# Optimization experiments

Hardware: AMD Instinct MI355X
Metric: run time of the kernel (lower is better)

Reference implementation:

```python
import jax, jax.numpy as jnp
import numpy as np

R = 8
INPUT_DIM = 2048
OUTPUT_DIM = 2048
SCALING = 16.0 / R  # lora_alpha / r
TEMPERATURE = 1.0
LN_EPS = 1e-5


def setup_inputs() -> dict:
    key = jax.random.key(0)
    ks = jax.random.split(key, 6)
    bs, seq, ctr_out, ctr_final = 8, 2048, 32, 4
    x = jax.random.normal(ks[0], (bs, seq, INPUT_DIM), dtype=jnp.float32)
    ctr = jax.random.normal(ks[1], (bs, ctr_out), dtype=jnp.float32)
    W1 = jax.random.normal(ks[2], (60, ctr_out), dtype=jnp.float32) * (1.0 / np.sqrt(ctr_out))
    b1 = jnp.zeros((60,), jnp.float32)
    W2 = jax.random.normal(ks[3], (ctr_final, 60), dtype=jnp.float32) * (1.0 / np.sqrt(60))
    b2 = jnp.zeros((ctr_final,), jnp.float32)
    Wa = jax.random.normal(ks[4], (INPUT_DIM * R, ctr_final), dtype=jnp.float32) * 0.02
    Wb = jax.random.normal(ks[5], (R * OUTPUT_DIM, ctr_final), dtype=jnp.float32) * 0.02
    return {
        'x': x, 'ctr_hidden_states': ctr,
        'ln_gamma': jnp.ones((ctr_out,), jnp.float32),
        'ln_beta': jnp.zeros((ctr_out,), jnp.float32),
        'W1': W1, 'b1': b1, 'W2': W2, 'b2': b2, 'Wa': Wa, 'Wb': Wb,
    }


def reference(x, ctr_hidden_states, ln_gamma, ln_beta, W1, b1, W2, b2, Wa, Wb):
    bs = x.shape[0]
    # gating MLP (default which_in_gate branch): LN -> Linear -> ReLU -> Linear
    mu = jnp.mean(ctr_hidden_states, axis=-1, keepdims=True)
    var = jnp.mean(jnp.square(ctr_hidden_states - mu), axis=-1, keepdims=True)
    z = (ctr_hidden_states - mu) * jax.lax.rsqrt(var + LN_EPS) * ln_gamma + ln_beta
    h = jax.nn.relu(z @ W1.T + b1)                 # [bs, 60]
    gate = h @ W2.T + b2                           # [bs, ctr_final_dim]
    # soft routing with softmax
    gate = jax.nn.softmax(gate / TEMPERATURE, axis=-1)
    # per-sample low-rank adapters
    A = (gate @ Wa.T).reshape(bs, R, INPUT_DIM)    # [bs, r, d_in]
    B = (gate @ Wb.T).reshape(bs, R, OUTPUT_DIM)   # [bs, r, d_out]
    # out = (x @ A^T) @ B * scaling
    xa = jnp.einsum('bsd,brd->bsr', x, A)          # [bs, seq, r]
    out = jnp.einsum('bsr,bro->bso', xa, B) * SCALING
    return out
```

## Files before the change

### kernel.cpp

```cpp
#include <hip/hip_runtime.h>
#include <hip/hip_bf16.h>
#include <math.h>


#define BS 8
#define SEQ 2048
#define DIM 2048
#define RR 8
#define SCALING 2.0f

__global__ void gate_ab_kernel(const float* __restrict__ ctr,
                               const float* __restrict__ gamma,
                               const float* __restrict__ beta,
                               const float* __restrict__ W1,
                               const float* __restrict__ b1,
                               const float* __restrict__ W2,
                               const float* __restrict__ b2,
                               const float* __restrict__ Wa,
                               const float* __restrict__ Wb,
                               float* __restrict__ A,
                               float* __restrict__ B) {
    __shared__ float z_s[BS][32];
    __shared__ float h_s[BS][60];
    __shared__ float logit_s[BS][4];
    __shared__ float gate_s[BS][4];
    const int tid = threadIdx.x;

    {
        const int b = tid >> 5, i = tid & 31;
        float v = ctr[b * 32 + i];
        float s = v;
        #pragma unroll
        for (int m = 16; m; m >>= 1) s += __shfl_xor(s, m, 64);
        const float mu = s * (1.0f / 32.0f);
        const float d = v - mu;
        float sq = d * d;
        #pragma unroll
        for (int m = 16; m; m >>= 1) sq += __shfl_xor(sq, m, 64);
        const float var = sq * (1.0f / 32.0f);
        z_s[b][i] = d * rsqrtf(var + 1e-5f) * gamma[i] + beta[i];
    }
    __syncthreads();

    for (int idx = tid; idx < BS * 60; idx += 256) {
        const int b = idx / 60, j = idx % 60;
        float acc = b1[j];
        #pragma unroll
        for (int k = 0; k < 32; ++k) acc += z_s[b][k] * W1[j * 32 + k];
        h_s[b][j] = fmaxf(acc, 0.0f);
    }
    __syncthreads();

    if (tid < 32) {
        const int b = tid >> 2, c = tid & 3;
        float acc = b2[c];
        for (int k = 0; k < 60; ++k) acc += h_s[b][k] * W2[c * 60 + k];
        logit_s[b][c] = acc;
    }
    __syncthreads();

    if (tid < 8) {
        float m = logit_s[tid][0];
        #pragma unroll
        for (int c = 1; c < 4; ++c) m = fmaxf(m, logit_s[tid][c]);
        float e[4], s = 0.0f;
        #pragma unroll
        for (int c = 0; c < 4; ++c) { e[c] = expf(logit_s[tid][c] - m); s += e[c]; }
        const float inv = 1.0f / s;
        #pragma unroll
        for (int c = 0; c < 4; ++c) gate_s[tid][c] = e[c] * inv;
    }
    __syncthreads();

    const float4* __restrict__ Wa4 = (const float4*)Wa;
    const float4* __restrict__ Wb4 = (const float4*)Wb;
    const int total = BS * RR * DIM;
    for (int idx = blockIdx.x * 256 + tid; idx < total; idx += gridDim.x * 256) {
        const int b = idx >> 14, rd = idx & 16383;
        const float4 g = *(const float4*)gate_s[b];
        const float4 wa = Wa4[rd];
        A[idx] = g.x * wa.x + g.y * wa.y + g.z * wa.z + g.w * wa.w;
        const float4 wb = Wb4[rd];
        B[idx] = SCALING * (g.x * wb.x + g.y * wb.y + g.z * wb.z + g.w * wb.w);
    }
}

__global__ void __launch_bounds__(512, 4)
fused_kernel(const float* __restrict__ x, const float* __restrict__ A,
             const float* __restrict__ B, float* __restrict__ out) {
    __shared__ float Ts[RR * DIM];
    const int b = blockIdx.x >> 6;
    const int tile = blockIdx.x & 63;
    const int wave = threadIdx.x >> 6, lane = threadIdx.x & 63;

    {
        const float4* __restrict__ src = (const float4*)(A + b * (RR * DIM));
        float4* dst = (float4*)Ts;
        for (int i = threadIdx.x; i < RR * DIM / 4; i += 512) dst[i] = src[i];
    }
    __syncthreads();

    const float* __restrict__ xr =
        x + ((size_t)b * SEQ + tile * 32 + wave * 4) * DIM;

    float acc[4][8];
    #pragma unroll
    for (int i = 0; i < 4; ++i)
        #pragma unroll
        for (int r = 0; r < 8; ++r) acc[i][r] = 0.0f;

    float4 xcur[4], xnxt[4];
    {
        const int d0 = lane * 4;
        #pragma unroll
        for (int i = 0; i < 4; ++i)
            xcur[i] = *(const float4*)&xr[(size_t)i * DIM + d0];
    }
    #pragma unroll
    for (int j = 0; j < 8; ++j) {
        const int d = j * 256 + lane * 4;
        if (j < 7) {
            #pragma unroll
            for (int i = 0; i < 4; ++i)
                xnxt[i] = *(const float4*)&xr[(size_t)i * DIM + d + 256];
        }
        float4 a4[8];
        #pragma unroll
        for (int r = 0; r < 8; ++r) a4[r] = *(const float4*)&Ts[r * DIM + d];
        #pragma unroll
        for (int i = 0; i < 4; ++i) {
            #pragma unroll
            for (int r = 0; r < 8; ++r)
                acc[i][r] += xcur[i].x * a4[r].x + xcur[i].y * a4[r].y +
                             xcur[i].z * a4[r].z + xcur[i].w * a4[r].w;
        }
        #pragma unroll
        for (int i = 0; i < 4; ++i) xcur[i] = xnxt[i];
    }

    float xa[4][8];
    #pragma unroll
    for (int i = 0; i < 4; ++i) {
        #pragma unroll
        for (int r = 0; r < 8; ++r) {
            float v = acc[i][r];
            #pragma unroll
            for (int off = 32; off; off >>= 1) v += __shfl_xor(v, off, 64);
            xa[i][r] = v;
        }
    }

    __syncthreads();
    {
        const float4* __restrict__ src = (const float4*)(B + b * (RR * DIM));
        float4* dst = (float4*)Ts;
        for (int i = threadIdx.x; i < RR * DIM / 4; i += 512) dst[i] = src[i];
    }
    __syncthreads();

    float* __restrict__ ob =
        out + ((size_t)b * SEQ + tile * 32 + wave * 4) * DIM;
    #pragma unroll
    for (int j = 0; j < 8; ++j) {
        const int o = j * 256 + lane * 4;
        float4 b4[8];
        #pragma unroll
        for (int r = 0; r < 8; ++r) b4[r] = *(const float4*)&Ts[r * DIM + o];
        #pragma unroll
        for (int i = 0; i < 4; ++i) {
            float4 v = {0.0f, 0.0f, 0.0f, 0.0f};
            #pragma unroll
            for (int r = 0; r < 8; ++r) {
                v.x += xa[i][r] * b4[r].x;
                v.y += xa[i][r] * b4[r].y;
                v.z += xa[i][r] * b4[r].z;
                v.w += xa[i][r] * b4[r].w;
            }
            *(float4*)&ob[(size_t)i * DIM + o] = v;
        }
    }
}

extern "C" void kernel_launch(void* const* d_in, const int* in_sizes, int n_in,
                              void* d_out, int out_size, void* d_ws, size_t ws_size,
                              hipStream_t stream) {
    const float* x     = (const float*)d_in[0];
    const float* ctr   = (const float*)d_in[1];
    const float* gamma = (const float*)d_in[2];
    const float* beta  = (const float*)d_in[3];
    const float* W1    = (const float*)d_in[4];
    const float* b1    = (const float*)d_in[5];
    const float* W2    = (const float*)d_in[6];
    const float* b2    = (const float*)d_in[7];
    const float* Wa    = (const float*)d_in[8];
    const float* Wb    = (const float*)d_in[9];

    float* ws = (float*)d_ws;
    float* A  = ws;
    float* B  = ws + 131072;
    float* out = (float*)d_out;

    gate_ab_kernel<<<128, 256, 0, stream>>>(ctr, gamma, beta, W1, b1, W2, b2,
                                            Wa, Wb, A, B);
    fused_kernel<<<BS * 64, 512, 0, stream>>>(x, A, B, out);
}
```

Baseline: 259.0 us.

## Read A/B adapters directly from global memory and shrink blocks to two rows per wave

Removes the shared-memory staging of the per-batch A and B matrices, along with the two block barriers. The kernel now reads A and B straight from global memory, relying on L2 and L1 caching since every block reuses the same 64KB per batch. Blocks shrink from 512 to 256 threads, each wave handles 2 rows instead of 4, and the grid grows to 2048 blocks to raise occupancy. The trade-off is more cache traffic for A and B per row and less reuse of each loaded A/B vector across rows.

```diff
diff --git a/kernel.cpp b/kernel.cpp
--- a/kernel.cpp
+++ b/kernel.cpp
@@ -85,96 +85,77 @@
     }
 }
 
-__global__ void __launch_bounds__(512, 4)
+__global__ void __launch_bounds__(256, 6)
 fused_kernel(const float* __restrict__ x, const float* __restrict__ A,
              const float* __restrict__ B, float* __restrict__ out) {
-    __shared__ float Ts[RR * DIM];
-    const int b = blockIdx.x >> 6;
-    const int tile = blockIdx.x & 63;
+    const int b = blockIdx.x >> 8;
+    const int tile = blockIdx.x & 255;
     const int wave = threadIdx.x >> 6, lane = threadIdx.x & 63;
+    const int row = tile * 8 + wave * 2;
 
-    {
-        const float4* __restrict__ src = (const float4*)(A + b * (RR * DIM));
-        float4* dst = (float4*)Ts;
-        for (int i = threadIdx.x; i < RR * DIM / 4; i += 512) dst[i] = src[i];
-    }
-    __syncthreads();
+    const float* __restrict__ Ag = A + b * (RR * DIM);
+    const float* __restrict__ Bg = B + b * (RR * DIM);
+    const float* __restrict__ xr = x + ((size_t)b * SEQ + row) * DIM;
 
-    const float* __restrict__ xr =
-        x + ((size_t)b * SEQ + tile * 32 + wave * 4) * DIM;
-
-    float acc[4][8];
+    float acc[2][8];
     #pragma unroll
-    for (int i = 0; i < 4; ++i)
+    for (int i = 0; i < 2; ++i)
         #pragma unroll
         for (int r = 0; r < 8; ++r) acc[i][r] = 0.0f;
 
-    float4 xcur[4], xnxt[4];
+    float4 xc[2], xn[2];
     {
         const int d0 = lane * 4;
-        #pragma unroll
-        for (int i = 0; i < 4; ++i)
-            xcur[i] = *(const float4*)&xr[(size_t)i * DIM + d0];
+        xc[0] = *(const float4*)&xr[d0];
+        xc[1] = *(const float4*)&xr[DIM + d0];
     }
     #pragma unroll
     for (int j = 0; j < 8; ++j) {
         const int d = j * 256 + lane * 4;
         if (j < 7) {
-            #pragma unroll
-            for (int i = 0; i < 4; ++i)
-                xnxt[i] = *(const float4*)&xr[(size_t)i * DIM + d + 256];
+            xn[0] = *(const float4*)&xr[d + 256];
+            xn[1] = *(const float4*)&xr[DIM + d + 256];
         }
         float4 a4[8];
         #pragma unroll
-        for (int r = 0; r < 8; ++r) a4[r] = *(const float4*)&Ts[r * DIM + d];
+        for (int r = 0; r < 8; ++r) a4[r] = *(const float4*)&Ag[r * DIM + d];
         #pragma unroll
-        for (int i = 0; i < 4; ++i) {
+        for (int i = 0; i < 2; ++i) {
             #pragma unroll
             for (int r = 0; r < 8; ++r)
-                acc[i][r] += xcur[i].x * a4[r].x + xcur[i].y * a4[r].y +
-                             xcur[i].z * a4[r].z + xcur[i].w * a4[r].w;
+                acc[i][r] += xc[i].x * a4[r].x + xc[i].y * a4[r].y +
+                             xc[i].z * a4[r].z + xc[i].w * a4[r].w;
         }
-        #pragma unroll
-        for (int i = 0; i < 4; ++i) xcur[i] = xnxt[i];
+        xc[0] = xn[0];
+        xc[1] = xn[1];
     }
 
-    float xa[4][8];
     #pragma unroll
-    for (int i = 0; i < 4; ++i) {
+    for (int i = 0; i < 2; ++i)
         #pragma unroll
         for (int r = 0; r < 8; ++r) {
             float v = acc[i][r];
             #pragma unroll
             for (int off = 32; off; off >>= 1) v += __shfl_xor(v, off, 64);
-            xa[i][r] = v;
+            acc[i][r] = v;
         }
-    }
 
-    __syncthreads();
-    {
-        const float4* __restrict__ src = (const float4*)(B + b * (RR * DIM));
-        float4* dst = (float4*)Ts;
-        for (int i = threadIdx.x; i < RR * DIM / 4; i += 512) dst[i] = src[i];
-    }
-    __syncthreads();
-
-    float* __restrict__ ob =
-        out + ((size_t)b * SEQ + tile * 32 + wave * 4) * DIM;
+    float* __restrict__ ob = out + ((size_t)b * SEQ + row) * DIM;
     #pragma unroll
     for (int j = 0; j < 8; ++j) {
         const int o = j * 256 + lane * 4;
         float4 b4[8];
         #pragma unroll
-        for (int r = 0; r < 8; ++r) b4[r] = *(const float4*)&Ts[r * DIM + o];
+        for (int r = 0; r < 8; ++r) b4[r] = *(const float4*)&Bg[r * DIM + o];
         #pragma unroll
-        for (int i = 0; i < 4; ++i) {
+        for (int i = 0; i < 2; ++i) {
             float4 v = {0.0f, 0.0f, 0.0f, 0.0f};
             #pragma unroll
             for (int r = 0; r < 8; ++r) {
-                v.x += xa[i][r] * b4[r].x;
-                v.y += xa[i][r] * b4[r].y;
-                v.z += xa[i][r] * b4[r].z;
-                v.w += xa[i][r] * b4[r].w;
+                v.x += acc[i][r] * b4[r].x;
+                v.y += acc[i][r] * b4[r].y;
+                v.z += acc[i][r] * b4[r].z;
+                v.w += acc[i][r] * b4[r].w;
             }
             *(float4*)&ob[(size_t)i * DIM + o] = v;
         }
@@ -202,5 +183,5 @@
 
     gate_ab_kernel<<<128, 256, 0, stream>>>(ctr, gamma, beta, W1, b1, W2, b2,
                                             Wa, Wb, A, B);
-    fused_kernel<<<BS * 64, 512, 0, stream>>>(x, A, B, out);
+    fused_kernel<<<2048, 256, 0, stream>>>(x, A, B, out);
 }
```

Result: slower. 430.3 us (+66.1%).
